# Kernel optimization log

Hardware: AMD Instinct MI355X
Metric: run time of the kernel (lower is better)

## Reference

```python
import jax, jax.numpy as jnp
import numpy as np

K = 3  # dcn kernel size
PAD = (K - 1) // 2
GRAD_MUL = 0.1


def _deform_conv(x, offsets, weight):
    """DCNv1 (no modulation), stride 1, padding PAD, deformable_groups=1.
    x: [B,C,H,W]; offsets: [B,2*K*K,H,W] with (y,x) pairs per kernel point;
    weight: [O,C,K,K]. Returns [B,O,H,W].
    """
    B, C, H, W = x.shape
    K2 = K * K
    off = offsets.reshape(B, K2, 2, H, W)
    base = jnp.arange(K, dtype=x.dtype) - PAD            # [-1, 0, 1]
    base_y = jnp.repeat(base, K)                          # y repeated
    base_x = jnp.tile(base, K)                            # x tiled
    # sampling coordinates: p0 + pk + offset  -> [B,K2,H,W]
    py = jnp.arange(H, dtype=x.dtype)[None, None, :, None] + base_y[None, :, None, None] + off[:, :, 0]
    px = jnp.arange(W, dtype=x.dtype)[None, None, None, :] + base_x[None, :, None, None] + off[:, :, 1]
    y0 = jnp.floor(py)
    x0 = jnp.floor(px)
    ly = py - y0
    lx = px - x0
    y0i = y0.astype(jnp.int32)
    x0i = x0.astype(jnp.int32)
    x_flat = x.reshape(B, C, H * W)

    def corner(yy, xx, w):
        valid = (yy >= 0) & (yy < H) & (xx >= 0) & (xx < W)
        idx = jnp.clip(yy, 0, H - 1) * W + jnp.clip(xx, 0, W - 1)  # [B,K2,H,W]
        g = jax.vmap(lambda xf, ix: jnp.take(xf, ix.reshape(-1), axis=1))(x_flat, idx)
        g = g.reshape(B, C, K2, H, W)
        return g * (w * valid.astype(x.dtype))[:, None]

    sampled = (corner(y0i, x0i, (1 - ly) * (1 - lx))
               + corner(y0i, x0i + 1, (1 - ly) * lx)
               + corner(y0i + 1, x0i, ly * (1 - lx))
               + corner(y0i + 1, x0i + 1, ly * lx))  # [B,C,K2,H,W]
    w_r = weight.reshape(weight.shape[0], C, K2)
    return jnp.einsum('bckhw,ock->bohw', sampled, w_r)


def setup_inputs() -> dict:
    key = jax.random.key(0)
    k1, k2, k3 = jax.random.split(key, 3)
    B, C, H, W, O = 4, 256, 64, 64, 256
    x = jax.random.normal(k1, (B, C, H, W), dtype=jnp.float32)
    shape_pred = jax.random.normal(k2, (B, 2 * K * K, H, W), dtype=jnp.float32)
    weight = jax.random.normal(k3, (O, C, K, K), dtype=jnp.float32) * 0.01  # normal_init std=0.01
    return {"x": x, "shape_pred": shape_pred, "weight": weight}


def reference(x, shape_pred, weight):
    base = jnp.arange(K, dtype=x.dtype) - PAD
    # dcn_base_offset: (y,x) pairs per kernel point, flattened -> [2*K*K]
    dcn_base = jnp.stack([jnp.repeat(base, K), jnp.tile(base, K)], axis=1).reshape(-1)
    sp = shape_pred * GRAD_MUL + jax.lax.stop_gradient(shape_pred) * (1.0 - GRAD_MUL)
    dcn_offset = sp - dcn_base[None, :, None, None]
    return jax.nn.relu(_deform_conv(x, dcn_offset, weight))
```

## Files before the change

### kernel.cpp

```cpp
#include <hip/hip_runtime.h>
#include <hip/hip_bf16.h>

#define BB 4
#define CC 256
#define HH 64
#define WW 64
#define OO 256
#define NK2 9
#define HWP (HH*WW)
#define KD (NK2*CC)
#define PART_ELEMS (BB*OO*HWP)
#define XT_BYTES   8388608ull
#define WT_BYTES   1179648ull
#define PART_OFF   (XT_BYTES + WT_BYTES)

typedef __bf16 bf16x8 __attribute__((ext_vector_type(8)));
typedef float f32x4 __attribute__((ext_vector_type(4)));
typedef float f32x8 __attribute__((ext_vector_type(8)));
typedef unsigned short u16x8 __attribute__((ext_vector_type(8)));

static __device__ __forceinline__ float bf2f(unsigned short v) {
  return __uint_as_float(((unsigned)v) << 16);
}
static __device__ __forceinline__ unsigned short f2bf(float f) {
  __hip_bfloat16 h = __float2bfloat16(f);
  return __builtin_bit_cast(unsigned short, h);
}

__global__ void k_xpose(const float* __restrict__ x, unsigned short* __restrict__ xt) {
  __shared__ float tile[32][33];
  int b  = blockIdx.z;
  int c0 = blockIdx.y * 32;
  int p0 = blockIdx.x * 32;
  int tx = threadIdx.x & 31;
  int ty = threadIdx.x >> 5;
  const float* src = x + ((size_t)b * CC + c0) * HWP + p0;
#pragma unroll
  for (int i = 0; i < 4; ++i)
    tile[ty + i * 8][tx] = src[(size_t)(ty + i * 8) * HWP + tx];
  __syncthreads();
  unsigned short* dst = xt + ((size_t)b * HWP + p0) * CC + c0;
#pragma unroll
  for (int i = 0; i < 4; ++i) {
    float v = tile[tx][ty + i * 8];
    dst[(size_t)(ty + i * 8) * CC + tx] = f2bf(v);
  }
}

__global__ void k_wt(const float* __restrict__ w, unsigned short* __restrict__ wt) {
  int i = blockIdx.x * 256 + threadIdx.x;
  if (i >= OO * KD) return;
  int kpt = i >> 16;
  int rem = i & 65535;
  int kk = rem >> 13;
  int rem2 = rem & 8191;
  int o = rem2 >> 5;
  int f = rem2 & 31;
  int c = kk * 32 + f;
  wt[i] = f2bf(w[((size_t)o * CC + c) * NK2 + kpt]);
}

template<int KPTN, int NG, int BF16OUT>
__launch_bounds__(512)
__global__ void k_dcn(const unsigned short* __restrict__ xt,
                      const unsigned short* __restrict__ wt,
                      const float* __restrict__ sp,
                      void* __restrict__ dstv) {
  __shared__ __align__(16) unsigned short Alds[128 * 256];

  const int tid = threadIdx.x;
  constexpr int NBLK = NG * BB * (HH / 2);
  const int hw = blockIdx.x;
  const int swz = (hw & 7) * (NBLK / 8) + (hw >> 3);
  const int g = swz % NG;
  const int rest = swz / NG;
  const int y0 = (rest & 31) * 2;
  const int b = rest >> 5;
  const int kpt0 = g * KPTN;

  const int t8 = tid & 7;
  const int pxb = tid >> 3;

  const int wv = tid >> 6;
  const int lane = tid & 63;
  const int l15 = lane & 15;
  const int lg = lane >> 4;
  const int obase = wv * 32;

  float offY[2][KPTN], offX[2][KPTN];
#pragma unroll
  for (int h = 0; h < 2; ++h)
#pragma unroll
    for (int t = 0; t < KPTN; ++t) {
      offY[h][t] = sp[((size_t)b * 18 + 2 * (kpt0 + t)) * HWP + (y0 + h) * WW + pxb];
      offX[h][t] = sp[((size_t)b * 18 + 2 * (kpt0 + t) + 1) * HWP + (y0 + h) * WW + pxb];
    }

  f32x4 acc[2][8];
#pragma unroll
  for (int i = 0; i < 2; ++i)
#pragma unroll
    for (int j = 0; j < 8; ++j)
      acc[i][j] = (f32x4){0.f, 0.f, 0.f, 0.f};

  const unsigned short* wbase[2];
#pragma unroll
  for (int fm = 0; fm < 2; ++fm)
    wbase[fm] = wt + (size_t)(obase + fm * 16 + l15) * 32 + lg * 8;

  char* Ab = (char*)Alds;
  const unsigned short* xb = xt + (size_t)b * HWP * CC;

#pragma unroll
  for (int t = 0; t < KPTN; ++t) {
    const int kpt = kpt0 + t;
#pragma unroll
    for (int h = 0; h < 2; ++h) {
      const int pm = h * 64 + pxb;
      float py = (float)(y0 + h) + offY[h][t];
      float pxx = (float)pxb + offX[h][t];
      float fy = floorf(py), fx = floorf(pxx);
      float ly = py - fy, lx = pxx - fx;
      int y0i = (int)fy, x0i = (int)fx;
      int y1i = y0i + 1, x1i = x0i + 1;
      bool vy0 = (y0i >= 0) & (y0i < HH);
      bool vy1 = (y1i >= 0) & (y1i < HH);
      bool vx0 = (x0i >= 0) & (x0i < WW);
      bool vx1 = (x1i >= 0) & (x1i < WW);
      float w00 = (1.f - ly) * (1.f - lx);
      float w01 = (1.f - ly) * lx;
      float w10 = ly * (1.f - lx);
      float w11 = ly * lx;
      w00 = (vy0 && vx0) ? w00 : 0.f;
      w01 = (vy0 && vx1) ? w01 : 0.f;
      w10 = (vy1 && vx0) ? w10 : 0.f;
      w11 = (vy1 && vx1) ? w11 : 0.f;
      int yc0 = min(max(y0i, 0), HH - 1), yc1 = min(max(y1i, 0), HH - 1);
      int xc0 = min(max(x0i, 0), WW - 1), xc1 = min(max(x1i, 0), WW - 1);
      const unsigned short* p00 = xb + (yc0 * WW + xc0) * CC + t8 * 8;
      const unsigned short* p01 = xb + (yc0 * WW + xc1) * CC + t8 * 8;
      const unsigned short* p10 = xb + (yc1 * WW + xc0) * CC + t8 * 8;
      const unsigned short* p11 = xb + (yc1 * WW + xc1) * CC + t8 * 8;
#pragma unroll
      for (int cg = 0; cg < 4; ++cg) {
        u16x8 a00 = *reinterpret_cast<const u16x8*>(p00 + cg * 64);
        u16x8 a01 = *reinterpret_cast<const u16x8*>(p01 + cg * 64);
        u16x8 a10 = *reinterpret_cast<const u16x8*>(p10 + cg * 64);
        u16x8 a11 = *reinterpret_cast<const u16x8*>(p11 + cg * 64);
        u16x8 r;
#pragma unroll
        for (int j = 0; j < 8; ++j) {
          float s = fmaf(w11, bf2f(a11[j]),
                    fmaf(w10, bf2f(a10[j]),
                    fmaf(w01, bf2f(a01[j]), w00 * bf2f(a00[j]))));
          r[j] = f2bf(s);
        }
        unsigned bo = (unsigned)(pm * 512 + cg * 128 + t8 * 16) ^ (unsigned)((pm & 7) << 4);
        *reinterpret_cast<u16x8*>(Ab + bo) = r;
      }
    }
    __syncthreads();

#define LOADK(AF, BF, KK)                                                          \
    {                                                                              \
      _Pragma("unroll")                                                            \
      for (int fm = 0; fm < 2; ++fm)                                               \
        AF[fm] = __builtin_bit_cast(bf16x8,                                        \
            *reinterpret_cast<const u16x8*>(wbase[fm] + (size_t)(kpt * 8 + (KK)) * 8192)); \
      _Pragma("unroll")                                                            \
      for (int fn = 0; fn < 8; ++fn) {                                             \
        int mr = fn * 16 + l15;                                                    \
        unsigned bo = (unsigned)(mr * 512 + (KK) * 64 + lg * 16) ^ (unsigned)((mr & 7) << 4); \
        BF[fn] = __builtin_bit_cast(bf16x8, *reinterpret_cast<const u16x8*>(Ab + bo)); \
      }                                                                            \
    }
#define DOMFMA(AF, BF)                                                             \
    {                                                                              \
      _Pragma("unroll")                                                            \
      for (int fm = 0; fm < 2; ++fm)                                               \
        _Pragma("unroll")                                                          \
        for (int fn = 0; fn < 8; ++fn)                                             \
          acc[fm][fn] = __builtin_amdgcn_mfma_f32_16x16x32_bf16(AF[fm], BF[fn], acc[fm][fn], 0, 0, 0); \
    }
    {
      bf16x8 a0[2], a1[2];
      bf16x8 b0[8], b1[8];
      LOADK(a0, b0, 0);
#pragma unroll
      for (int kk = 0; kk < 8; ++kk) {
        if ((kk & 1) == 0) {
          if (kk < 7) LOADK(a1, b1, kk + 1);
          DOMFMA(a0, b0);
        } else {
          if (kk < 7) LOADK(a0, b0, kk + 1);
          DOMFMA(a1, b1);
        }
      }
    }
    __syncthreads();
  }

#pragma unroll
  for (int fm = 0; fm < 2; ++fm) {
#pragma unroll
    for (int fn = 0; fn < 8; ++fn) {
#pragma unroll
      for (int r = 0; r < 4; ++r) {
        int o = obase + fm * 16 + lg * 4 + r;
        int m = fn * 16 + l15;
        int yy = y0 + (m >> 6);
        int xx = m & 63;
        size_t idx = (((size_t)b * OO + o) * HH + yy) * WW + xx;
        float v = acc[fm][fn][r];
        if (BF16OUT) {
          ((unsigned short*)dstv)[(size_t)g * PART_ELEMS + idx] = f2bf(v);
        } else {
          ((float*)dstv)[idx] = fmaxf(v, 0.0f);
        }
      }
    }
  }
}

__global__ void k_reduce(const unsigned short* __restrict__ parts, float* __restrict__ out, int n8) {
  int i = blockIdx.x * 256 + threadIdx.x;
  if (i >= n8) return;
  const u16x8* p0 = (const u16x8*)parts;
  const u16x8* p1 = p0 + (PART_ELEMS / 8);
  const u16x8* p2 = p1 + (PART_ELEMS / 8);
  u16x8 a = p0[i], b = p1[i], c = p2[i];
  f32x8 o;
#pragma unroll
  for (int j = 0; j < 8; ++j)
    o[j] = fmaxf(bf2f(a[j]) + bf2f(b[j]) + bf2f(c[j]), 0.0f);
  *reinterpret_cast<f32x8*>(out + (size_t)i * 8) = o;
}

extern "C" void kernel_launch(void* const* d_in, const int* in_sizes, int n_in,
                              void* d_out, int out_size, void* d_ws, size_t ws_size,
                              hipStream_t stream) {
  const float* x = (const float*)d_in[0];
  const float* sp = (const float*)d_in[1];
  const float* w = (const float*)d_in[2];
  float* out = (float*)d_out;

  unsigned short* xt = (unsigned short*)d_ws;
  unsigned short* wt = (unsigned short*)((char*)d_ws + XT_BYTES);
  unsigned short* parts = (unsigned short*)((char*)d_ws + PART_OFF);

  k_xpose<<<dim3(HWP / 32, CC / 32, BB), 256, 0, stream>>>(x, xt);
  k_wt<<<(OO * KD + 255) / 256, 256, 0, stream>>>(w, wt);

  const size_t need = PART_OFF + 3ull * PART_ELEMS * sizeof(unsigned short);
  if (ws_size >= need) {
    k_dcn<3, 3, 1><<<3 * BB * (HH / 2), 512, 0, stream>>>(xt, wt, sp, parts);
    k_reduce<<<PART_ELEMS / 8 / 256, 256, 0, stream>>>(parts, out, PART_ELEMS / 8);
  } else {
    k_dcn<9, 1, 0><<<BB * (HH / 2), 512, 0, stream>>>(xt, wt, sp, out);
  }
}
```

Measured before the change: 60.32 us.

## Split channel dimension across blocks and reduce six bf16 partials

Each deformable-conv block now processes only half of the input channels, doubling the grid and halving the LDS tile per block. Partial outputs for each kernel-point group and channel half are written as bf16 and summed by a generalized reduce kernel. This aims for better CU occupancy and load balance, at the cost of double the partial-buffer traffic and more bf16 rounding of partial sums.

```diff
diff --git a/kernel.cpp b/kernel.cpp
--- a/kernel.cpp
+++ b/kernel.cpp
@@ -60,23 +60,30 @@
   wt[i] = f2bf(w[((size_t)o * CC + c) * NK2 + kpt]);
 }
 
-template<int KPTN, int NG, int BF16OUT>
+template<int KPTN, int NG, int CHN, int BF16OUT>
 __launch_bounds__(512)
 __global__ void k_dcn(const unsigned short* __restrict__ xt,
                       const unsigned short* __restrict__ wt,
                       const float* __restrict__ sp,
                       void* __restrict__ dstv) {
-  __shared__ __align__(16) unsigned short Alds[128 * 256];
+  constexpr int NKH = 256 / CHN;
+  constexpr int RS = CHN * 2;
+  constexpr int NCG = CHN / 64;
+  constexpr int NKK = CHN / 32;
+  __shared__ __align__(16) unsigned short Alds[128 * CHN];
 
   const int tid = threadIdx.x;
-  constexpr int NBLK = NG * BB * (HH / 2);
+  constexpr int NBLK = NG * NKH * BB * (HH / 2);
   const int hw = blockIdx.x;
   const int swz = (hw & 7) * (NBLK / 8) + (hw >> 3);
-  const int g = swz % NG;
-  const int rest = swz / NG;
+  const int gg = swz % (NG * NKH);
+  const int gk = gg / NKH;
+  const int kh = gg % NKH;
+  const int rest = swz / (NG * NKH);
   const int y0 = (rest & 31) * 2;
   const int b = rest >> 5;
-  const int kpt0 = g * KPTN;
+  const int kpt0 = gk * KPTN;
+  const int cb = kh * CHN;
 
   const int t8 = tid & 7;
   const int pxb = tid >> 3;
@@ -109,7 +116,7 @@
     wbase[fm] = wt + (size_t)(obase + fm * 16 + l15) * 32 + lg * 8;
 
   char* Ab = (char*)Alds;
-  const unsigned short* xb = xt + (size_t)b * HWP * CC;
+  const unsigned short* xb = xt + (size_t)b * HWP * CC + cb;
 
 #pragma unroll
   for (int t = 0; t < KPTN; ++t) {
@@ -142,7 +149,7 @@
       const unsigned short* p10 = xb + (yc1 * WW + xc0) * CC + t8 * 8;
       const unsigned short* p11 = xb + (yc1 * WW + xc1) * CC + t8 * 8;
 #pragma unroll
-      for (int cg = 0; cg < 4; ++cg) {
+      for (int cg = 0; cg < NCG; ++cg) {
         u16x8 a00 = *reinterpret_cast<const u16x8*>(p00 + cg * 64);
         u16x8 a01 = *reinterpret_cast<const u16x8*>(p01 + cg * 64);
         u16x8 a10 = *reinterpret_cast<const u16x8*>(p10 + cg * 64);
@@ -155,7 +162,7 @@
                     fmaf(w01, bf2f(a01[j]), w00 * bf2f(a00[j]))));
           r[j] = f2bf(s);
         }
-        unsigned bo = (unsigned)(pm * 512 + cg * 128 + t8 * 16) ^ (unsigned)((pm & 7) << 4);
+        unsigned bo = (unsigned)(pm * RS + cg * 128 + t8 * 16) ^ (unsigned)((pm & 7) << 4);
         *reinterpret_cast<u16x8*>(Ab + bo) = r;
       }
     }
@@ -166,11 +173,11 @@
       _Pragma("unroll")                                                            \
       for (int fm = 0; fm < 2; ++fm)                                               \
         AF[fm] = __builtin_bit_cast(bf16x8,                                        \
-            *reinterpret_cast<const u16x8*>(wbase[fm] + (size_t)(kpt * 8 + (KK)) * 8192)); \
+            *reinterpret_cast<const u16x8*>(wbase[fm] + (size_t)(kpt * 8 + kh * NKK + (KK)) * 8192)); \
       _Pragma("unroll")                                                            \
       for (int fn = 0; fn < 8; ++fn) {                                             \
         int mr = fn * 16 + l15;                                                    \
-        unsigned bo = (unsigned)(mr * 512 + (KK) * 64 + lg * 16) ^ (unsigned)((mr & 7) << 4); \
+        unsigned bo = (unsigned)(mr * RS + (KK) * 64 + lg * 16) ^ (unsigned)((mr & 7) << 4); \
         BF[fn] = __builtin_bit_cast(bf16x8, *reinterpret_cast<const u16x8*>(Ab + bo)); \
       }                                                                            \
     }
@@ -187,12 +194,12 @@
       bf16x8 b0[8], b1[8];
       LOADK(a0, b0, 0);
 #pragma unroll
-      for (int kk = 0; kk < 8; ++kk) {
+      for (int kk = 0; kk < NKK; ++kk) {
         if ((kk & 1) == 0) {
-          if (kk < 7) LOADK(a1, b1, kk + 1);
+          if (kk < NKK - 1) LOADK(a1, b1, kk + 1);
           DOMFMA(a0, b0);
         } else {
-          if (kk < 7) LOADK(a0, b0, kk + 1);
+          if (kk < NKK - 1) LOADK(a0, b0, kk + 1);
           DOMFMA(a1, b1);
         }
       }
@@ -213,7 +220,7 @@
         size_t idx = (((size_t)b * OO + o) * HH + yy) * WW + xx;
         float v = acc[fm][fn][r];
         if (BF16OUT) {
-          ((unsigned short*)dstv)[(size_t)g * PART_ELEMS + idx] = f2bf(v);
+          ((unsigned short*)dstv)[(size_t)gg * PART_ELEMS + idx] = f2bf(v);
         } else {
           ((float*)dstv)[idx] = fmaxf(v, 0.0f);
         }
@@ -222,17 +229,23 @@
   }
 }
 
-__global__ void k_reduce(const unsigned short* __restrict__ parts, float* __restrict__ out, int n8) {
+template<int NP>
+__global__ void k_reduceN(const unsigned short* __restrict__ parts, float* __restrict__ out, int n8) {
   int i = blockIdx.x * 256 + threadIdx.x;
   if (i >= n8) return;
-  const u16x8* p0 = (const u16x8*)parts;
-  const u16x8* p1 = p0 + (PART_ELEMS / 8);
-  const u16x8* p2 = p1 + (PART_ELEMS / 8);
-  u16x8 a = p0[i], b = p1[i], c = p2[i];
+  const u16x8* p = (const u16x8*)parts;
+  f32x8 s;
+#pragma unroll
+  for (int j = 0; j < 8; ++j) s[j] = 0.0f;
+#pragma unroll
+  for (int q = 0; q < NP; ++q) {
+    u16x8 v = p[i + (size_t)q * (PART_ELEMS / 8)];
+#pragma unroll
+    for (int j = 0; j < 8; ++j) s[j] += bf2f(v[j]);
+  }
   f32x8 o;
 #pragma unroll
-  for (int j = 0; j < 8; ++j)
-    o[j] = fmaxf(bf2f(a[j]) + bf2f(b[j]) + bf2f(c[j]), 0.0f);
+  for (int j = 0; j < 8; ++j) o[j] = fmaxf(s[j], 0.0f);
   *reinterpret_cast<f32x8*>(out + (size_t)i * 8) = o;
 }
 
@@ -251,11 +264,11 @@
   k_xpose<<<dim3(HWP / 32, CC / 32, BB), 256, 0, stream>>>(x, xt);
   k_wt<<<(OO * KD + 255) / 256, 256, 0, stream>>>(w, wt);
 
-  const size_t need = PART_OFF + 3ull * PART_ELEMS * sizeof(unsigned short);
+  const size_t need = PART_OFF + 6ull * PART_ELEMS * sizeof(unsigned short);
   if (ws_size >= need) {
-    k_dcn<3, 3, 1><<<3 * BB * (HH / 2), 512, 0, stream>>>(xt, wt, sp, parts);
-    k_reduce<<<PART_ELEMS / 8 / 256, 256, 0, stream>>>(parts, out, PART_ELEMS / 8);
+    k_dcn<3, 3, 128, 1><<<3 * 2 * BB * (HH / 2), 512, 0, stream>>>(xt, wt, sp, parts);
+    k_reduceN<6><<<PART_ELEMS / 8 / 256, 256, 0, stream>>>(parts, out, PART_ELEMS / 8);
   } else {
-    k_dcn<9, 1, 0><<<BB * (HH / 2), 512, 0, stream>>>(xt, wt, sp, out);
-  }
-}
+    k_dcn<9, 1, 256, 0><<<BB * (HH / 2), 512, 0, stream>>>(xt, wt, sp, out);
+  }
+}
```

Measured after the change: 63.75 us. 5.7% more time.

## Software-pipeline DCN gather with double-buffered half-channel LDS stages

Applied to the files above, without the earlier changes.

Splits the partial-sum DCN kernel into six half-channel (128-wide) stages with double-buffered LDS. Each stage's bilinear gather loads are issued before the previous stage's MFMA work, so global gather latency overlaps with matrix math. LDS use per block halves, which may allow more blocks per CU, but there are more barriers and higher register pressure from the in-flight gather registers. The fallback path is also rewritten as a non-templated kernel without A/B fragment double-buffering.

```diff
diff --git a/kernel.cpp b/kernel.cpp
--- a/kernel.cpp
+++ b/kernel.cpp
@@ -60,23 +60,21 @@
   wt[i] = f2bf(w[((size_t)o * CC + c) * NK2 + kpt]);
 }
 
-template<int KPTN, int NG, int BF16OUT>
 __launch_bounds__(512)
-__global__ void k_dcn(const unsigned short* __restrict__ xt,
-                      const unsigned short* __restrict__ wt,
-                      const float* __restrict__ sp,
-                      void* __restrict__ dstv) {
-  __shared__ __align__(16) unsigned short Alds[128 * 256];
+__global__ void k_dcn_p(const unsigned short* __restrict__ xt,
+                        const unsigned short* __restrict__ wt,
+                        const float* __restrict__ sp,
+                        unsigned short* __restrict__ parts) {
+  __shared__ __align__(16) unsigned short Alds[2][128 * 128];
 
   const int tid = threadIdx.x;
-  constexpr int NBLK = NG * BB * (HH / 2);
   const int hw = blockIdx.x;
-  const int swz = (hw & 7) * (NBLK / 8) + (hw >> 3);
-  const int g = swz % NG;
-  const int rest = swz / NG;
+  const int swz = (hw & 7) * 48 + (hw >> 3);
+  const int g = swz % 3;
+  const int rest = swz / 3;
   const int y0 = (rest & 31) * 2;
   const int b = rest >> 5;
-  const int kpt0 = g * KPTN;
+  const int kpt0 = g * 3;
 
   const int t8 = tid & 7;
   const int pxb = tid >> 3;
@@ -87,11 +85,11 @@
   const int lg = lane >> 4;
   const int obase = wv * 32;
 
-  float offY[2][KPTN], offX[2][KPTN];
+  float offY[2][3], offX[2][3];
 #pragma unroll
   for (int h = 0; h < 2; ++h)
 #pragma unroll
-    for (int t = 0; t < KPTN; ++t) {
+    for (int t = 0; t < 3; ++t) {
       offY[h][t] = sp[((size_t)b * 18 + 2 * (kpt0 + t)) * HWP + (y0 + h) * WW + pxb];
       offX[h][t] = sp[((size_t)b * 18 + 2 * (kpt0 + t) + 1) * HWP + (y0 + h) * WW + pxb];
     }
@@ -103,22 +101,191 @@
     for (int j = 0; j < 8; ++j)
       acc[i][j] = (f32x4){0.f, 0.f, 0.f, 0.f};
 
-  const unsigned short* wbase[2];
-#pragma unroll
-  for (int fm = 0; fm < 2; ++fm)
-    wbase[fm] = wt + (size_t)(obase + fm * 16 + l15) * 32 + lg * 8;
+  const unsigned short* xb = xt + (size_t)b * HWP * CC;
+
+  float w00, w01, w10, w11;
+  unsigned c00, c01, c10, c11;
+  u16x8 d0, d1, d2, d3, d4, d5, d6, d7;
+
+#define CALC(H, T)                                                             \
+  {                                                                            \
+    float py = (float)(y0 + (H)) + offY[H][T];                                 \
+    float px = (float)pxb + offX[H][T];                                        \
+    float fy = floorf(py), fx = floorf(px);                                    \
+    float ly = py - fy, lx = px - fx;                                          \
+    int y0i = (int)fy, x0i = (int)fx;                                          \
+    int y1i = y0i + 1, x1i = x0i + 1;                                          \
+    bool vy0 = (y0i >= 0) & (y0i < HH);                                        \
+    bool vy1 = (y1i >= 0) & (y1i < HH);                                        \
+    bool vx0 = (x0i >= 0) & (x0i < WW);                                        \
+    bool vx1 = (x1i >= 0) & (x1i < WW);                                        \
+    w00 = (1.f - ly) * (1.f - lx);                                             \
+    w01 = (1.f - ly) * lx;                                                     \
+    w10 = ly * (1.f - lx);                                                     \
+    w11 = ly * lx;                                                             \
+    w00 = (vy0 && vx0) ? w00 : 0.f;                                            \
+    w01 = (vy0 && vx1) ? w01 : 0.f;                                            \
+    w10 = (vy1 && vx0) ? w10 : 0.f;                                            \
+    w11 = (vy1 && vx1) ? w11 : 0.f;                                            \
+    int yc0 = min(max(y0i, 0), HH - 1), yc1 = min(max(y1i, 0), HH - 1);        \
+    int xc0 = min(max(x0i, 0), WW - 1), xc1 = min(max(x1i, 0), WW - 1);        \
+    c00 = (unsigned)((yc0 * WW + xc0) * CC);                                   \
+    c01 = (unsigned)((yc0 * WW + xc1) * CC);                                   \
+    c10 = (unsigned)((yc1 * WW + xc0) * CC);                                   \
+    c11 = (unsigned)((yc1 * WW + xc1) * CC);                                   \
+  }
+
+#define ISSUE(S)                                                               \
+  {                                                                            \
+    const unsigned short* q = xb + ((S) & 1) * 128 + t8 * 8;                   \
+    d0 = *reinterpret_cast<const u16x8*>(q + c00);                             \
+    d1 = *reinterpret_cast<const u16x8*>(q + c00 + 64);                        \
+    d2 = *reinterpret_cast<const u16x8*>(q + c01);                             \
+    d3 = *reinterpret_cast<const u16x8*>(q + c01 + 64);                        \
+    d4 = *reinterpret_cast<const u16x8*>(q + c10);                             \
+    d5 = *reinterpret_cast<const u16x8*>(q + c10 + 64);                        \
+    d6 = *reinterpret_cast<const u16x8*>(q + c11);                             \
+    d7 = *reinterpret_cast<const u16x8*>(q + c11 + 64);                        \
+  }
+
+#define BLEND(S, H)                                                            \
+  {                                                                            \
+    char* Bp = (char*)Alds[(S) & 1];                                           \
+    const int pm = (H) * 64 + pxb;                                             \
+    u16x8 r0, r1;                                                              \
+    _Pragma("unroll")                                                          \
+    for (int j = 0; j < 8; ++j) {                                              \
+      float s0 = fmaf(w11, bf2f(d6[j]), fmaf(w10, bf2f(d4[j]),                 \
+                 fmaf(w01, bf2f(d2[j]), w00 * bf2f(d0[j]))));                  \
+      float s1 = fmaf(w11, bf2f(d7[j]), fmaf(w10, bf2f(d5[j]),                 \
+                 fmaf(w01, bf2f(d3[j]), w00 * bf2f(d1[j]))));                  \
+      r0[j] = f2bf(s0);                                                        \
+      r1[j] = f2bf(s1);                                                        \
+    }                                                                          \
+    unsigned bo0 = (unsigned)(pm * 256 + t8 * 16) ^ (unsigned)((pm & 7) << 4); \
+    unsigned bo1 = (unsigned)(pm * 256 + 128 + t8 * 16) ^ (unsigned)((pm & 7) << 4); \
+    *reinterpret_cast<u16x8*>(Bp + bo0) = r0;                                  \
+    *reinterpret_cast<u16x8*>(Bp + bo1) = r1;                                  \
+  }
+
+#define MFMA_S(S, T)                                                           \
+  {                                                                            \
+    const char* Bp = (const char*)Alds[(S) & 1];                               \
+    _Pragma("unroll")                                                          \
+    for (int kk = 0; kk < 4; ++kk) {                                           \
+      bf16x8 afr[2], bfr[8];                                                   \
+      _Pragma("unroll")                                                        \
+      for (int fm = 0; fm < 2; ++fm)                                           \
+        afr[fm] = __builtin_bit_cast(bf16x8, *reinterpret_cast<const u16x8*>(  \
+            wt + (size_t)((kpt0 + (T)) * 8 + ((S) & 1) * 4 + kk) * 8192        \
+               + (obase + fm * 16 + l15) * 32 + lg * 8));                      \
+      _Pragma("unroll")                                                        \
+      for (int fn = 0; fn < 8; ++fn) {                                         \
+        int mr = fn * 16 + l15;                                                \
+        unsigned bo = (unsigned)(mr * 256 + kk * 64 + lg * 16) ^ (unsigned)((mr & 7) << 4); \
+        bfr[fn] = __builtin_bit_cast(bf16x8, *reinterpret_cast<const u16x8*>(Bp + bo)); \
+      }                                                                        \
+      _Pragma("unroll")                                                        \
+      for (int fm = 0; fm < 2; ++fm)                                           \
+        _Pragma("unroll")                                                      \
+        for (int fn = 0; fn < 8; ++fn)                                         \
+          acc[fm][fn] = __builtin_amdgcn_mfma_f32_16x16x32_bf16(afr[fm], bfr[fn], acc[fm][fn], 0, 0, 0); \
+    }                                                                          \
+  }
+
+  CALC(0, 0); ISSUE(0); BLEND(0, 0);
+  CALC(1, 0); ISSUE(0); BLEND(0, 1);
+  CALC(0, 0); ISSUE(1);
+  __syncthreads();
+
+  MFMA_S(0, 0);
+  BLEND(1, 0);
+  CALC(1, 0); ISSUE(1); BLEND(1, 1);
+  CALC(0, 1); ISSUE(2);
+  __syncthreads();
+
+  MFMA_S(1, 0);
+  BLEND(2, 0);
+  CALC(1, 1); ISSUE(2); BLEND(2, 1);
+  CALC(0, 1); ISSUE(3);
+  __syncthreads();
+
+  MFMA_S(2, 1);
+  BLEND(3, 0);
+  CALC(1, 1); ISSUE(3); BLEND(3, 1);
+  CALC(0, 2); ISSUE(4);
+  __syncthreads();
+
+  MFMA_S(3, 1);
+  BLEND(4, 0);
+  CALC(1, 2); ISSUE(4); BLEND(4, 1);
+  CALC(0, 2); ISSUE(5);
+  __syncthreads();
+
+  MFMA_S(4, 2);
+  BLEND(5, 0);
+  CALC(1, 2); ISSUE(5); BLEND(5, 1);
+  __syncthreads();
+
+  MFMA_S(5, 2);
+
+  unsigned short* dp = parts + (size_t)g * PART_ELEMS;
+#pragma unroll
+  for (int fm = 0; fm < 2; ++fm) {
+#pragma unroll
+    for (int fn = 0; fn < 8; ++fn) {
+#pragma unroll
+      for (int r = 0; r < 4; ++r) {
+        int o = obase + fm * 16 + lg * 4 + r;
+        int m = fn * 16 + l15;
+        int yy = y0 + (m >> 6);
+        int xx = m & 63;
+        dp[(((size_t)b * OO + o) * HH + yy) * WW + xx] = f2bf(acc[fm][fn][r]);
+      }
+    }
+  }
+}
+
+__launch_bounds__(512)
+__global__ void k_dcn_f(const unsigned short* __restrict__ xt,
+                        const unsigned short* __restrict__ wt,
+                        const float* __restrict__ sp,
+                        float* __restrict__ outp) {
+  __shared__ __align__(16) unsigned short Alds[128 * 256];
+
+  const int tid = threadIdx.x;
+  const int hw = blockIdx.x;
+  const int swz = (hw & 7) * 16 + (hw >> 3);
+  const int y0 = (swz & 31) * 2;
+  const int b = swz >> 5;
+
+  const int t8 = tid & 7;
+  const int pxb = tid >> 3;
+
+  const int wv = tid >> 6;
+  const int lane = tid & 63;
+  const int l15 = lane & 15;
+  const int lg = lane >> 4;
+  const int obase = wv * 32;
+
+  f32x4 acc[2][8];
+#pragma unroll
+  for (int i = 0; i < 2; ++i)
+#pragma unroll
+    for (int j = 0; j < 8; ++j)
+      acc[i][j] = (f32x4){0.f, 0.f, 0.f, 0.f};
 
   char* Ab = (char*)Alds;
   const unsigned short* xb = xt + (size_t)b * HWP * CC;
 
-#pragma unroll
-  for (int t = 0; t < KPTN; ++t) {
-    const int kpt = kpt0 + t;
+  for (int kpt = 0; kpt < NK2; ++kpt) {
 #pragma unroll
     for (int h = 0; h < 2; ++h) {
       const int pm = h * 64 + pxb;
-      float py = (float)(y0 + h) + offY[h][t];
-      float pxx = (float)pxb + offX[h][t];
+      float offY = sp[((size_t)b * 18 + 2 * kpt) * HWP + (y0 + h) * WW + pxb];
+      float offX = sp[((size_t)b * 18 + 2 * kpt + 1) * HWP + (y0 + h) * WW + pxb];
+      float py = (float)(y0 + h) + offY;
+      float pxx = (float)pxb + offX;
       float fy = floorf(py), fx = floorf(pxx);
       float ly = py - fy, lx = pxx - fx;
       int y0i = (int)fy, x0i = (int)fx;
@@ -161,41 +328,24 @@
     }
     __syncthreads();
 
-#define LOADK(AF, BF, KK)                                                          \
-    {                                                                              \
-      _Pragma("unroll")                                                            \
-      for (int fm = 0; fm < 2; ++fm)                                               \
-        AF[fm] = __builtin_bit_cast(bf16x8,                                        \
-            *reinterpret_cast<const u16x8*>(wbase[fm] + (size_t)(kpt * 8 + (KK)) * 8192)); \
-      _Pragma("unroll")                                                            \
-      for (int fn = 0; fn < 8; ++fn) {                                             \
-        int mr = fn * 16 + l15;                                                    \
-        unsigned bo = (unsigned)(mr * 512 + (KK) * 64 + lg * 16) ^ (unsigned)((mr & 7) << 4); \
-        BF[fn] = __builtin_bit_cast(bf16x8, *reinterpret_cast<const u16x8*>(Ab + bo)); \
-      }                                                                            \
-    }
-#define DOMFMA(AF, BF)                                                             \
-    {                                                                              \
-      _Pragma("unroll")                                                            \
-      for (int fm = 0; fm < 2; ++fm)                                               \
-        _Pragma("unroll")                                                          \
-        for (int fn = 0; fn < 8; ++fn)                                             \
-          acc[fm][fn] = __builtin_amdgcn_mfma_f32_16x16x32_bf16(AF[fm], BF[fn], acc[fm][fn], 0, 0, 0); \
-    }
-    {
-      bf16x8 a0[2], a1[2];
-      bf16x8 b0[8], b1[8];
-      LOADK(a0, b0, 0);
-#pragma unroll
-      for (int kk = 0; kk < 8; ++kk) {
-        if ((kk & 1) == 0) {
-          if (kk < 7) LOADK(a1, b1, kk + 1);
-          DOMFMA(a0, b0);
-        } else {
-          if (kk < 7) LOADK(a0, b0, kk + 1);
-          DOMFMA(a1, b1);
-        }
+#pragma unroll
+    for (int kk = 0; kk < 8; ++kk) {
+      bf16x8 afr[2], bfr[8];
+#pragma unroll
+      for (int fm = 0; fm < 2; ++fm)
+        afr[fm] = __builtin_bit_cast(bf16x8, *reinterpret_cast<const u16x8*>(
+            wt + (size_t)(kpt * 8 + kk) * 8192 + (obase + fm * 16 + l15) * 32 + lg * 8));
+#pragma unroll
+      for (int fn = 0; fn < 8; ++fn) {
+        int mr = fn * 16 + l15;
+        unsigned bo = (unsigned)(mr * 512 + kk * 64 + lg * 16) ^ (unsigned)((mr & 7) << 4);
+        bfr[fn] = __builtin_bit_cast(bf16x8, *reinterpret_cast<const u16x8*>(Ab + bo));
       }
+#pragma unroll
+      for (int fm = 0; fm < 2; ++fm)
+#pragma unroll
+        for (int fn = 0; fn < 8; ++fn)
+          acc[fm][fn] = __builtin_amdgcn_mfma_f32_16x16x32_bf16(afr[fm], bfr[fn], acc[fm][fn], 0, 0, 0);
     }
     __syncthreads();
   }
@@ -210,29 +360,29 @@
         int m = fn * 16 + l15;
         int yy = y0 + (m >> 6);
         int xx = m & 63;
-        size_t idx = (((size_t)b * OO + o) * HH + yy) * WW + xx;
-        float v = acc[fm][fn][r];
-        if (BF16OUT) {
-          ((unsigned short*)dstv)[(size_t)g * PART_ELEMS + idx] = f2bf(v);
-        } else {
-          ((float*)dstv)[idx] = fmaxf(v, 0.0f);
-        }
+        outp[(((size_t)b * OO + o) * HH + yy) * WW + xx] = fmaxf(acc[fm][fn][r], 0.0f);
       }
     }
   }
 }
 
-__global__ void k_reduce(const unsigned short* __restrict__ parts, float* __restrict__ out, int n8) {
+template<int NP>
+__global__ void k_reduceN(const unsigned short* __restrict__ parts, float* __restrict__ out, int n8) {
   int i = blockIdx.x * 256 + threadIdx.x;
   if (i >= n8) return;
-  const u16x8* p0 = (const u16x8*)parts;
-  const u16x8* p1 = p0 + (PART_ELEMS / 8);
-  const u16x8* p2 = p1 + (PART_ELEMS / 8);
-  u16x8 a = p0[i], b = p1[i], c = p2[i];
+  const u16x8* p = (const u16x8*)parts;
+  f32x8 s;
+#pragma unroll
+  for (int j = 0; j < 8; ++j) s[j] = 0.0f;
+#pragma unroll
+  for (int q = 0; q < NP; ++q) {
+    u16x8 v = p[i + (size_t)q * (PART_ELEMS / 8)];
+#pragma unroll
+    for (int j = 0; j < 8; ++j) s[j] += bf2f(v[j]);
+  }
   f32x8 o;
 #pragma unroll
-  for (int j = 0; j < 8; ++j)
-    o[j] = fmaxf(bf2f(a[j]) + bf2f(b[j]) + bf2f(c[j]), 0.0f);
+  for (int j = 0; j < 8; ++j) o[j] = fmaxf(s[j], 0.0f);
   *reinterpret_cast<f32x8*>(out + (size_t)i * 8) = o;
 }
 
@@ -253,9 +403,9 @@
 
   const size_t need = PART_OFF + 3ull * PART_ELEMS * sizeof(unsigned short);
   if (ws_size >= need) {
-    k_dcn<3, 3, 1><<<3 * BB * (HH / 2), 512, 0, stream>>>(xt, wt, sp, parts);
-    k_reduce<<<PART_ELEMS / 8 / 256, 256, 0, stream>>>(parts, out, PART_ELEMS / 8);
+    k_dcn_p<<<384, 512, 0, stream>>>(xt, wt, sp, parts);
+    k_reduceN<3><<<PART_ELEMS / 8 / 256, 256, 0, stream>>>(parts, out, PART_ELEMS / 8);
   } else {
-    k_dcn<9, 1, 0><<<BB * (HH / 2), 512, 0, stream>>>(xt, wt, sp, out);
-  }
-}
+    k_dcn_f<<<128, 512, 0, stream>>>(xt, wt, sp, out);
+  }
+}
```

Result: no change. 60.21 us (-0.2%).
